# Kernel tuning notes

Hardware: AMD Instinct MI355X
Metric: run time of the kernel (lower is better)

The kernel has to match this reference:

```python
import jax, jax.numpy as jnp
import numpy as np

SEQ_LEN, IN_DIM = 120, 132
UNITS = (64, 128, 64)
N_LABELS = 101


def _lstm(x, W, U, b):
    """Keras-style LSTM with activation='relu', recurrent_activation='sigmoid'.
    x: (B,T,D), W: (D,4u), U: (u,4u), b: (4u,). Gate order i,f,c,o.
    Returns full hidden sequence (B,T,u)."""
    u = U.shape[0]
    # precompute input projections for all timesteps (big GEMM outside scan)
    xz = jnp.einsum('btd,dz->btz', x, W) + b  # (B,T,4u)

    def step(carry, z_t):
        h, c = carry
        z = z_t + h @ U  # (B,4u)
        i, f, g, o = jnp.split(z, 4, axis=-1)
        i = jax.nn.sigmoid(i)
        f = jax.nn.sigmoid(f)
        o = jax.nn.sigmoid(o)
        c = f * c + i * jax.nn.relu(g)
        h = o * jax.nn.relu(c)
        return (h, c), h

    B = x.shape[0]
    h0 = jnp.zeros((B, u), x.dtype)
    (_, _), hs = jax.lax.scan(step, (h0, h0), jnp.swapaxes(xz, 0, 1))
    return jnp.swapaxes(hs, 0, 1)  # (B,T,u)


def setup_inputs() -> dict:
    key = jax.random.key(0)
    ks = jax.random.split(key, 16)
    s = 0.05
    d = {'x': jax.random.normal(ks[0], (1024, SEQ_LEN, IN_DIM), jnp.float32)}
    in_dims = (IN_DIM,) + UNITS[:-1]
    for l, (din, u) in enumerate(zip(in_dims, UNITS), start=1):
        d[f'W{l}'] = jax.random.normal(ks[3 * l - 2], (din, 4 * u), jnp.float32) * s
        d[f'U{l}'] = jax.random.normal(ks[3 * l - 1], (u, 4 * u), jnp.float32) * s
        d[f'b{l}'] = jnp.zeros((4 * u,), jnp.float32)
    dense_dims = [(UNITS[-1], 64), (64, 32), (32, N_LABELS)]
    for l, (din, dout) in enumerate(dense_dims, start=1):
        d[f'Wd{l}'] = jax.random.normal(ks[9 + l], (din, dout), jnp.float32) * s
        d[f'bd{l}'] = jnp.zeros((dout,), jnp.float32)
    return d


def reference(x, W1, U1, b1, W2, U2, b2, W3, U3, b3,
              Wd1, bd1, Wd2, bd2, Wd3, bd3):
    h = _lstm(x, W1, U1, b1)          # (B,T,64)
    h = _lstm(h, W2, U2, b2)          # (B,T,128)
    h = _lstm(h, W3, U3, b3)[:, -1]   # return_sequences=False -> (B,64)
    h = jax.nn.relu(h @ Wd1 + bd1)    # (B,64)
    h = jax.nn.relu(h @ Wd2 + bd2)    # (B,32)
    return jax.nn.softmax(h @ Wd3 + bd3, axis=-1)  # (B,101)
```

## Files before the change

kernel.cpp:

```cpp
#include <hip/hip_runtime.h>
#include <math.h>

#define T_STEPS 120
#define BATCH   1024

typedef __attribute__((ext_vector_type(8))) short bf16x8;
typedef __attribute__((ext_vector_type(4))) float f32x4;
typedef unsigned short u16;

__device__ __forceinline__ unsigned split2(float f) {
    union { float f; unsigned u; } a; a.f = f;
    unsigned hi = a.u >> 16;
    union { float f; unsigned u; } h; h.u = a.u & 0xFFFF0000u;
    union { float f; unsigned u; } b; b.f = f - h.f;
    unsigned rr = b.u + 0x7FFFu + ((b.u >> 16) & 1);
    return (hi << 16) | (rr >> 16);
}

__device__ __forceinline__ short bf16rne(float f) {
    union { float f; unsigned u; } a; a.f = f;
    unsigned r = a.u + 0x7FFFu + ((a.u >> 16) & 1);
    return (short)(r >> 16);
}

__device__ __forceinline__ float fast_sigmoid(float x) {
    float e = __expf(-x);
    return __builtin_amdgcn_rcpf(1.f + e);
}

__device__ __forceinline__ void block_sync_lds() {
    asm volatile("s_waitcnt lgkmcnt(0)" ::: "memory");
    __builtin_amdgcn_sched_barrier(0);
    __builtin_amdgcn_s_barrier();
    __builtin_amdgcn_sched_barrier(0);
}

__global__ __launch_bounds__(256)
void xconv(const float* __restrict__ x, u16* __restrict__ xhi)
{
    int idx = blockIdx.x * 256 + threadIdx.x;
    int k   = idx % 144;
    int bt  = idx / 144;
    float f = (k < 132) ? x[(size_t)bt * 132 + k] : 0.f;
    xhi[idx] = (u16)(unsigned short)bf16rne(f);
}

template<int U, int KXD, int KTX, int KTAIL, bool XLO, bool WLO, bool LAST_ONLY>
__global__ __launch_bounds__(512, 1)
void lstm_fused(const u16* __restrict__ xhi, const u16* __restrict__ xlo,
                const float* __restrict__ W, int KIN,
                const float* __restrict__ Uw, const float* __restrict__ bias,
                u16* __restrict__ hhi, u16* __restrict__ hlo,
                float* __restrict__ hlast)
{
    constexpr int NZ  = 4 * U;
    constexpr int KTH = U / 32;
    constexpr int NB  = 16;
    constexpr int HPLANE = NB * U;
    constexpr int NGRP = U / 16;
    constexpr int XPSTRIDE = 20;
    static_assert(NGRP * 128 == 512, "4 h-waves + 4 x-waves");

    __shared__ u16 hsh[4 * HPLANE];
    __shared__ float xp[2 * NZ * XPSTRIDE];

    const int tid  = threadIdx.x;
    const int lane = tid & 63;
    const int wid  = tid >> 6;
    const int ln   = lane & 15;
    const int lq   = lane >> 4;
    const bool ish = (wid < NGRP);
    const int g    = ish ? wid : wid - NGRP;
    const int unit = g * 16 + ln;
    const int b0   = blockIdx.x * NB;

    if (ish) {
        bf16x8 bwu[4][KTH];
#pragma unroll
        for (int p = 0; p < 4; ++p)
#pragma unroll
            for (int kt = 0; kt < KTH; ++kt)
#pragma unroll
                for (int e = 0; e < 8; ++e) {
                    int k = kt * 32 + lq * 8 + e;
                    bwu[p][kt][e] = bf16rne(Uw[(size_t)k * NZ + p * U + unit]);
                }
        float breg[4];
#pragma unroll
        for (int p = 0; p < 4; ++p) breg[p] = bias[p * U + unit];

        u16* hw0 = hsh + ((unit >> 3) * NB + lq * 4) * 8 + (unit & 7);
        u16* hw1 = hw0 + 2 * HPLANE;
        float creg[4];
#pragma unroll
        for (int r = 0; r < 4; ++r) {
            creg[r] = 0.f;
            hw0[r * 8] = 0;
            hw0[HPLANE + r * 8] = 0;
        }

        const u16* hrd[2][KTH];
#pragma unroll
        for (int b = 0; b < 2; ++b)
#pragma unroll
            for (int kt = 0; kt < KTH; ++kt)
                hrd[b][kt] = hsh + b * 2 * HPLANE + ((kt * 4 + lq) * NB + ln) * 8;

        const float* xprd[2];
        xprd[0] = xp;
        xprd[1] = xp + (size_t)NZ * XPSTRIDE;

        size_t ho = ((size_t)(b0 + lq * 4) * T_STEPS) * U + unit;

        block_sync_lds();

#define HSTEP(CUR, OTH, tc)                                                     \
    {                                                                           \
        f32x4 xpv[4];                                                           \
        _Pragma("unroll")                                                       \
        for (int p = 0; p < 4; ++p)                                             \
            xpv[p] = *reinterpret_cast<const f32x4*>(                           \
                xprd[CUR] + (p * U + unit) * XPSTRIDE + lq * 4);                \
        f32x4 acc[4] = {};                                                      \
        _Pragma("unroll")                                                       \
        for (int kt = 0; kt < KTH; ++kt) {                                      \
            bf16x8 ahh = *reinterpret_cast<const bf16x8*>(hrd[CUR][kt]);        \
            bf16x8 ahl = *reinterpret_cast<const bf16x8*>(hrd[CUR][kt] + HPLANE); \
            _Pragma("unroll")                                                   \
            for (int p = 0; p < 4; ++p) {                                       \
                acc[p] = __builtin_amdgcn_mfma_f32_16x16x32_bf16(ahh, bwu[p][kt], acc[p], 0, 0, 0); \
                acc[p] = __builtin_amdgcn_mfma_f32_16x16x32_bf16(ahl, bwu[p][kt], acc[p], 0, 0, 0); \
            }                                                                   \
        }                                                                       \
        _Pragma("unroll")                                                       \
        for (int r = 0; r < 4; ++r) {                                           \
            float zi = acc[0][r] + xpv[0][r] + breg[0];                         \
            float zf = acc[1][r] + xpv[1][r] + breg[1];                         \
            float zg = acc[2][r] + xpv[2][r] + breg[2];                         \
            float zo = acc[3][r] + xpv[3][r] + breg[3];                         \
            float si = fast_sigmoid(zi);                                        \
            float sf = fast_sigmoid(zf);                                        \
            float gg = fmaxf(zg, 0.f);                                          \
            float so = fast_sigmoid(zo);                                        \
            float c  = sf * creg[r] + si * gg;                                  \
            creg[r] = c;                                                        \
            float h = so * fmaxf(c, 0.f);                                       \
            unsigned s = split2(h);                                             \
            u16* hw = (OTH) ? hw1 : hw0;                                        \
            hw[r * 8] = (u16)(s >> 16);                                         \
            hw[HPLANE + r * 8] = (u16)s;                                        \
            if constexpr (!LAST_ONLY) {                                         \
                size_t o = ho + (size_t)r * (T_STEPS * U) + (size_t)(tc) * U;   \
                hhi[o] = (u16)(s >> 16);                                        \
                if constexpr (WLO) hlo[o] = (u16)s;                             \
            } else {                                                            \
                if ((tc) == T_STEPS - 1)                                        \
                    hlast[(size_t)(b0 + lq * 4 + r) * U + unit] = h;            \
            }                                                                   \
        }                                                                       \
        block_sync_lds();                                                       \
    }

        for (int t = 0; t < T_STEPS; t += 2) {
            HSTEP(0, 1, t)
            HSTEP(1, 0, t + 1)
        }
#undef HSTEP
    } else {
        bf16x8 wxw[KTX][4];
#pragma unroll
        for (int kt = 0; kt < KTX; ++kt)
#pragma unroll
            for (int p = 0; p < 4; ++p)
#pragma unroll
                for (int e = 0; e < 8; ++e) {
                    int k = kt * 32 + lq * 8 + e;
                    wxw[kt][p][e] = (k < KIN) ? bf16rne(W[(size_t)k * NZ + p * U + unit])
                                              : (short)0;
                }

        const u16* pxh = xhi + ((size_t)(b0 + ln) * T_STEPS) * KXD + lq * 8;
        const u16* pxl = XLO ? (xlo + ((size_t)(b0 + ln) * T_STEPS) * KXD + lq * 8) : nullptr;

        float* xpw[2];
        xpw[0] = xp;
        xpw[1] = xp + (size_t)NZ * XPSTRIDE;

        bf16x8 xfh[KTX] = {}, xfl[KTX] = {};
#pragma unroll
        for (int kt = 0; kt < KTX; ++kt)
            if (kt < KTX - 1 || lq < KTAIL) {
                xfh[kt] = *reinterpret_cast<const bf16x8*>(pxh + kt * 32);
                if constexpr (XLO)
                    xfl[kt] = *reinterpret_cast<const bf16x8*>(pxl + kt * 32);
            }

        {
            f32x4 xacc[4] = {};
#pragma unroll
            for (int kt = 0; kt < KTX; ++kt)
#pragma unroll
                for (int p = 0; p < 4; ++p) {
                    xacc[p] = __builtin_amdgcn_mfma_f32_16x16x32_bf16(xfh[kt], wxw[kt][p], xacc[p], 0, 0, 0);
                    if constexpr (XLO)
                        xacc[p] = __builtin_amdgcn_mfma_f32_16x16x32_bf16(xfl[kt], wxw[kt][p], xacc[p], 0, 0, 0);
                }
#pragma unroll
            for (int p = 0; p < 4; ++p)
                *reinterpret_cast<f32x4*>(xpw[0] + (p * U + unit) * XPSTRIDE + lq * 4) = xacc[p];
            pxh += KXD; if constexpr (XLO) pxl += KXD;
#pragma unroll
            for (int kt = 0; kt < KTX; ++kt)
                if (kt < KTX - 1 || lq < KTAIL) {
                    xfh[kt] = *reinterpret_cast<const bf16x8*>(pxh + kt * 32);
                    if constexpr (XLO)
                        xfl[kt] = *reinterpret_cast<const bf16x8*>(pxl + kt * 32);
                }
        }

        block_sync_lds();

#define XSTEP(OTH, tc)                                                          \
    {                                                                           \
        if ((tc) + 1 < T_STEPS) {                                               \
            f32x4 xacc[4] = {};                                                 \
            _Pragma("unroll")                                                   \
            for (int kt = 0; kt < KTX; ++kt)                                    \
            _Pragma("unroll")                                                   \
            for (int p = 0; p < 4; ++p) {                                       \
                xacc[p] = __builtin_amdgcn_mfma_f32_16x16x32_bf16(xfh[kt], wxw[kt][p], xacc[p], 0, 0, 0); \
                if constexpr (XLO)                                              \
                    xacc[p] = __builtin_amdgcn_mfma_f32_16x16x32_bf16(xfl[kt], wxw[kt][p], xacc[p], 0, 0, 0); \
            }                                                                   \
            _Pragma("unroll")                                                   \
            for (int p = 0; p < 4; ++p)                                         \
                *reinterpret_cast<f32x4*>(xpw[OTH] + (p * U + unit) * XPSTRIDE + lq * 4) = xacc[p]; \
            if ((tc) + 2 < T_STEPS) {                                           \
                pxh += KXD; if constexpr (XLO) pxl += KXD;                      \
                _Pragma("unroll")                                               \
                for (int kt = 0; kt < KTX; ++kt)                                \
                    if (kt < KTX - 1 || lq < KTAIL) {                           \
                        xfh[kt] = *reinterpret_cast<const bf16x8*>(pxh + kt * 32); \
                        if constexpr (XLO)                                      \
                            xfl[kt] = *reinterpret_cast<const bf16x8*>(pxl + kt * 32); \
                    }                                                           \
            }                                                                   \
        }                                                                       \
        block_sync_lds();                                                       \
    }

        for (int t = 0; t < T_STEPS; t += 2) {
            XSTEP(1, t)
            XSTEP(0, t + 1)
        }
#undef XSTEP
    }
}

__global__ __launch_bounds__(512, 1)
void lstm_l2(const u16* __restrict__ xhi,
             const float* __restrict__ W,
             const float* __restrict__ Uw,
             const float* __restrict__ bias,
             u16* __restrict__ hhi, u16* __restrict__ hlo)
{
    constexpr int U = 128, NZ = 512, KTH = 4, NB = 16, KXD = 64, KTX = 2;
    constexpr int HPLANE = NB * U;
    __shared__ u16 hsh[4 * HPLANE];
    __shared__ u16 Wl[KXD * NZ];

    const int tid  = threadIdx.x;
    const int lane = tid & 63;
    const int wid  = tid >> 6;
    const int ln   = lane & 15;
    const int lq   = lane >> 4;
    const int unit = wid * 16 + ln;
    const int b0   = blockIdx.x * NB;

    for (int idx = tid; idx < KXD * NZ; idx += 512) {
        int k = idx >> 9, n = idx & (NZ - 1);
        Wl[((k >> 3) * NZ + n) * 8 + (k & 7)] = (u16)bf16rne(W[(size_t)k * NZ + n]);
    }

    bf16x8 bwu[4][KTH];
#pragma unroll
    for (int p = 0; p < 4; ++p)
#pragma unroll
        for (int kt = 0; kt < KTH; ++kt)
#pragma unroll
            for (int e = 0; e < 8; ++e) {
                int k = kt * 32 + lq * 8 + e;
                bwu[p][kt][e] = bf16rne(Uw[(size_t)k * NZ + p * U + unit]);
            }
    float breg[4];
#pragma unroll
    for (int p = 0; p < 4; ++p) breg[p] = bias[p * U + unit];

    u16* hw0 = hsh + ((unit >> 3) * NB + lq * 4) * 8 + (unit & 7);
    u16* hw1 = hw0 + 2 * HPLANE;
    float creg[4];
#pragma unroll
    for (int r = 0; r < 4; ++r) {
        creg[r] = 0.f;
        hw0[r * 8] = 0;
        hw0[HPLANE + r * 8] = 0;
    }

    const u16* hrd[2][KTH];
#pragma unroll
    for (int b = 0; b < 2; ++b)
#pragma unroll
        for (int kt = 0; kt < KTH; ++kt)
            hrd[b][kt] = hsh + b * 2 * HPLANE + ((kt * 4 + lq) * NB + ln) * 8;

    const u16* wb = Wl + ((size_t)lq * NZ + unit) * 8;

    const u16* pxh = xhi + ((size_t)(b0 + ln) * T_STEPS) * KXD + lq * 8;
    bf16x8 xfh[KTX];
#pragma unroll
    for (int kt = 0; kt < KTX; ++kt)
        xfh[kt] = *reinterpret_cast<const bf16x8*>(pxh + kt * 32);

    size_t ho = ((size_t)(b0 + lq * 4) * T_STEPS) * U + unit;

    block_sync_lds();

#define L2STEP(CUR, OTH, tc)                                                    \
    {                                                                           \
        f32x4 acc[4] = {};                                                      \
        _Pragma("unroll")                                                       \
        for (int kt = 0; kt < KTH; ++kt) {                                      \
            bf16x8 ahh = *reinterpret_cast<const bf16x8*>(hrd[CUR][kt]);        \
            bf16x8 ahl = *reinterpret_cast<const bf16x8*>(hrd[CUR][kt] + HPLANE); \
            _Pragma("unroll")                                                   \
            for (int p = 0; p < 4; ++p) {                                       \
                acc[p] = __builtin_amdgcn_mfma_f32_16x16x32_bf16(ahh, bwu[p][kt], acc[p], 0, 0, 0); \
                acc[p] = __builtin_amdgcn_mfma_f32_16x16x32_bf16(ahl, bwu[p][kt], acc[p], 0, 0, 0); \
            }                                                                   \
        }                                                                       \
        _Pragma("unroll")                                                       \
        for (int kt = 0; kt < KTX; ++kt)                                        \
        _Pragma("unroll")                                                       \
        for (int p = 0; p < 4; ++p) {                                           \
            bf16x8 wf = *reinterpret_cast<const bf16x8*>(wb + (kt * 4 * NZ + p * U) * 8); \
            acc[p] = __builtin_amdgcn_mfma_f32_16x16x32_bf16(xfh[kt], wf, acc[p], 0, 0, 0); \
        }                                                                       \
        if ((tc) + 1 < T_STEPS) {                                               \
            pxh += KXD;                                                         \
            _Pragma("unroll")                                                   \
            for (int kt = 0; kt < KTX; ++kt)                                    \
                xfh[kt] = *reinterpret_cast<const bf16x8*>(pxh + kt * 32);      \
        }                                                                       \
        _Pragma("unroll")                                                       \
        for (int r = 0; r < 4; ++r) {                                           \
            float si = fast_sigmoid(acc[0][r] + breg[0]);                       \
            float sf = fast_sigmoid(acc[1][r] + breg[1]);                       \
            float gg = fmaxf(acc[2][r] + breg[2], 0.f);                         \
            float so = fast_sigmoid(acc[3][r] + breg[3]);                       \
            float c  = sf * creg[r] + si * gg;                                  \
            creg[r] = c;                                                        \
            float h = so * fmaxf(c, 0.f);                                       \
            unsigned s = split2(h);                                             \
            u16* hw = (OTH) ? hw1 : hw0;                                        \
            hw[r * 8] = (u16)(s >> 16);                                         \
            hw[HPLANE + r * 8] = (u16)s;                                        \
            size_t o = ho + (size_t)r * (T_STEPS * U) + (size_t)(tc) * U;       \
            hhi[o] = (u16)(s >> 16);                                            \
            hlo[o] = (u16)s;                                                    \
        }                                                                       \
        block_sync_lds();                                                       \
    }

    for (int t = 0; t < T_STEPS; t += 2) {
        L2STEP(0, 1, t)
        L2STEP(1, 0, t + 1)
    }
#undef L2STEP
}

__global__ __launch_bounds__(256)
void dense_head(const float* __restrict__ h3,
                const float* __restrict__ Wd1, const float* __restrict__ bd1,
                const float* __restrict__ Wd2, const float* __restrict__ bd2,
                const float* __restrict__ Wd3, const float* __restrict__ bd3,
                float* __restrict__ out)
{
    __shared__ float s1[4][64];
    __shared__ float s2[4][32];
    const int w    = threadIdx.x >> 6;
    const int lane = threadIdx.x & 63;
    const int row  = blockIdx.x * 4 + w;

    float hval = h3[(size_t)row * 64 + lane];
    float a = bd1[lane];
#pragma unroll
    for (int k = 0; k < 64; ++k) {
        float hk = __shfl(hval, k, 64);
        a = fmaf(hk, Wd1[k * 64 + lane], a);
    }
    s1[w][lane] = fmaxf(a, 0.f);
    __syncthreads();

    if (lane < 32) {
        float a2 = bd2[lane];
#pragma unroll
        for (int k = 0; k < 64; ++k) a2 = fmaf(s1[w][k], Wd2[k * 32 + lane], a2);
        s2[w][lane] = fmaxf(a2, 0.f);
    }
    __syncthreads();

    float a0 = bd3[lane];
#pragma unroll
    for (int k = 0; k < 32; ++k) a0 = fmaf(s2[w][k], Wd3[k * 101 + lane], a0);
    float a1 = -INFINITY;
    if (lane < 37) {
        a1 = bd3[64 + lane];
#pragma unroll
        for (int k = 0; k < 32; ++k) a1 = fmaf(s2[w][k], Wd3[k * 101 + 64 + lane], a1);
    }

    float m = fmaxf(a0, a1);
#pragma unroll
    for (int off = 32; off > 0; off >>= 1) m = fmaxf(m, __shfl_xor(m, off, 64));
    float e0 = expf(a0 - m);
    float e1 = (lane < 37) ? expf(a1 - m) : 0.f;
    float s = e0 + e1;
#pragma unroll
    for (int off = 32; off > 0; off >>= 1) s += __shfl_xor(s, off, 64);

    out[(size_t)row * 101 + lane] = e0 / s;
    if (lane < 37) out[(size_t)row * 101 + 64 + lane] = e1 / s;
}

extern "C" void kernel_launch(void* const* d_in, const int* in_sizes, int n_in,
                              void* d_out, int out_size, void* d_ws, size_t ws_size,
                              hipStream_t stream) {
    const float* x   = (const float*)d_in[0];
    const float* W1  = (const float*)d_in[1];
    const float* U1  = (const float*)d_in[2];
    const float* b1  = (const float*)d_in[3];
    const float* W2  = (const float*)d_in[4];
    const float* U2  = (const float*)d_in[5];
    const float* b2  = (const float*)d_in[6];
    const float* W3  = (const float*)d_in[7];
    const float* U3  = (const float*)d_in[8];
    const float* b3  = (const float*)d_in[9];
    const float* Wd1 = (const float*)d_in[10];
    const float* bd1 = (const float*)d_in[11];
    const float* Wd2 = (const float*)d_in[12];
    const float* bd2 = (const float*)d_in[13];
    const float* Wd3 = (const float*)d_in[14];
    const float* bd3 = (const float*)d_in[15];

    u16* ws16 = (u16*)d_ws;
    u16* xhi  = ws16;
    u16* h2hi = ws16;
    u16* h2lo = h2hi + 15728640;
    u16* h1hi = ws16 + 35389440;
    float* h3 = (float*)(ws16 + 51118080);

    xconv<<<(BATCH * T_STEPS * 144) / 256, 256, 0, stream>>>(x, xhi);
    lstm_fused<64, 144, 5, 2, false, false, false><<<64, 512, 0, stream>>>(
        xhi, nullptr, W1, 132, U1, b1, h1hi, nullptr, nullptr);
    lstm_l2<<<64, 512, 0, stream>>>(h1hi, W2, U2, b2, h2hi, h2lo);
    lstm_fused<64, 128, 4, 4, true, true, true><<<64, 512, 0, stream>>>(
        h2hi, h2lo, W3, 128, U3, b3, nullptr, nullptr, h3);
    dense_head<<<BATCH / 4, 256, 0, stream>>>(h3, Wd1, bd1, Wd2, bd2, Wd3, bd3,
                                              (float*)d_out);
}
```

Before: 507.6 us.

## Hoist input projections into standalone GEMM and drop split-bf16 precision

Moves the input projection of LSTM layers 1 and 3 out of the recurrent kernel into a separate MFMA GEMM that writes bf16 pre-activations in a step-major tiled layout. The recurrent kernel then only does the h@U recurrence, with 8 waves covering two 16-row batch tiles per block over 32 blocks. The hi/lo split-bf16 trick for h is removed in all layers, halving the recurrent MFMAs and h stores. In exchange the change adds a large xz round-trip through memory and lowers numerical precision (bf16 h and bf16 stored projections).

Result: slower. 538.7 us (+6.1%).

```diff
diff --git a/kernel.cpp b/kernel.cpp
--- a/kernel.cpp
+++ b/kernel.cpp
@@ -6,21 +6,20 @@
 
 typedef __attribute__((ext_vector_type(8))) short bf16x8;
 typedef __attribute__((ext_vector_type(4))) float f32x4;
+typedef __attribute__((ext_vector_type(4))) unsigned short us4;
 typedef unsigned short u16;
 
-__device__ __forceinline__ unsigned split2(float f) {
-    union { float f; unsigned u; } a; a.f = f;
-    unsigned hi = a.u >> 16;
-    union { float f; unsigned u; } h; h.u = a.u & 0xFFFF0000u;
-    union { float f; unsigned u; } b; b.f = f - h.f;
-    unsigned rr = b.u + 0x7FFFu + ((b.u >> 16) & 1);
-    return (hi << 16) | (rr >> 16);
-}
-
-__device__ __forceinline__ short bf16rne(float f) {
+__device__ __forceinline__ int gsw(int r) { return (r & 7) ^ ((r >> 3) & 1); }
+
+__device__ __forceinline__ u16 bf16rne(float f) {
     union { float f; unsigned u; } a; a.f = f;
     unsigned r = a.u + 0x7FFFu + ((a.u >> 16) & 1);
-    return (short)(r >> 16);
+    return (u16)(r >> 16);
+}
+
+__device__ __forceinline__ float bf2f(u16 v) {
+    union { unsigned u; float f; } a; a.u = ((unsigned)v) << 16;
+    return a.f;
 }
 
 __device__ __forceinline__ float fast_sigmoid(float x) {
@@ -35,109 +34,210 @@
     __builtin_amdgcn_sched_barrier(0);
 }
 
-__global__ __launch_bounds__(256)
-void xconv(const float* __restrict__ x, u16* __restrict__ xhi)
+template<bool AF32>
+__global__ __launch_bounds__(256, 2)
+void gemm_xz(const void* __restrict__ Av, const float* __restrict__ Bw,
+             u16* __restrict__ XZF, int N, int K)
 {
-    int idx = blockIdx.x * 256 + threadIdx.x;
-    int k   = idx % 144;
-    int bt  = idx / 144;
-    float f = (k < 132) ? x[(size_t)bt * 132 + k] : 0.f;
-    xhi[idx] = (u16)(unsigned short)bf16rne(f);
-}
-
-template<int U, int KXD, int KTX, int KTAIL, bool XLO, bool WLO, bool LAST_ONLY>
+    constexpr int BM = 128, BN = 64, BK = 64;
+    __shared__ u16 Ah[BM * BK];
+    __shared__ u16 Bh[BN * BK];
+
+    const float* Af = (const float*)Av;
+    const u16*   Ab = (const u16*)Av;
+
+    const int tid  = threadIdx.x;
+    const int lane = tid & 63;
+    const int wv   = tid >> 6;
+    const int wm   = wv & 1;
+    const int wn   = wv >> 1;
+    const int m0   = blockIdx.x * BM;
+    const int n0   = blockIdx.y * BN;
+
+    f32x4 acc[4][2] = {};
+
+    const int ktiles = (K + BK - 1) / BK;
+    for (int kt = 0; kt < ktiles; ++kt) {
+        const int kb = kt * BK;
+        __syncthreads();
+
+        {
+            const int f4   = tid & 15;
+            const int sub  = (f4 & 1) * 4;
+            const int k8   = f4 >> 1;
+            const int kidx = kb + f4 * 4;
+            const bool kok = (kidx < K);
+            for (int rd = 0; rd < 8; ++rd) {
+                int m  = rd * 16 + (tid >> 4);
+                int gm = m0 + m;
+                us4 hh;
+                if (kok) {
+                    if constexpr (AF32) {
+                        float4 v = *reinterpret_cast<const float4*>(
+                            &Af[(size_t)gm * K + kidx]);
+                        hh.x = bf16rne(v.x); hh.y = bf16rne(v.y);
+                        hh.z = bf16rne(v.z); hh.w = bf16rne(v.w);
+                    } else {
+                        hh = *reinterpret_cast<const us4*>(
+                            &Ab[(size_t)gm * K + kidx]);
+                    }
+                } else {
+                    hh.x = 0; hh.y = 0; hh.z = 0; hh.w = 0;
+                }
+                int off = m * 64 + ((k8 ^ gsw(m & 15)) * 8) + sub;
+                *reinterpret_cast<us4*>(&Ah[off]) = hh;
+            }
+        }
+        {
+#pragma unroll
+            for (int i = 0; i < 2; ++i) {
+                int u  = tid + i * 256;
+                int n  = u & 63;
+                int k8 = u >> 6;
+                u16 th[8];
+#pragma unroll
+                for (int e = 0; e < 8; ++e) {
+                    int k = kb + k8 * 8 + e;
+                    th[e] = (k < K) ? bf16rne(Bw[(size_t)k * N + n0 + n]) : (u16)0;
+                }
+                us4 h0, h1;
+                h0.x = th[0]; h0.y = th[1]; h0.z = th[2]; h0.w = th[3];
+                h1.x = th[4]; h1.y = th[5]; h1.z = th[6]; h1.w = th[7];
+                int off = n * 64 + ((k8 ^ gsw(n & 15)) * 8);
+                *reinterpret_cast<us4*>(&Bh[off])     = h0;
+                *reinterpret_cast<us4*>(&Bh[off + 4]) = h1;
+            }
+        }
+        __syncthreads();
+
+        const int row = lane & 15;
+        const int kq  = lane >> 4;
+        const int gr  = gsw(row);
+#pragma unroll
+        for (int ks = 0; ks < 2; ++ks) {
+            const int k8 = ks * 4 + kq;
+            bf16x8 bh[2];
+#pragma unroll
+            for (int ni = 0; ni < 2; ++ni) {
+                int n = wn * 32 + ni * 16 + row;
+                bh[ni] = *reinterpret_cast<const bf16x8*>(&Bh[n * 64 + ((k8 ^ gr) * 8)]);
+            }
+#pragma unroll
+            for (int mi = 0; mi < 4; ++mi) {
+                int m = wm * 64 + mi * 16 + row;
+                bf16x8 ah = *reinterpret_cast<const bf16x8*>(&Ah[m * 64 + ((k8 ^ gr) * 8)]);
+#pragma unroll
+                for (int ni = 0; ni < 2; ++ni)
+                    acc[mi][ni] = __builtin_amdgcn_mfma_f32_16x16x32_bf16(ah, bh[ni], acc[mi][ni], 0, 0, 0);
+            }
+        }
+    }
+
+    const int col = lane & 15;
+    const int rq  = (lane >> 4) * 4;
+#pragma unroll
+    for (int mi = 0; mi < 4; ++mi) {
+#pragma unroll
+        for (int r = 0; r < 4; ++r) {
+            int gm = m0 + wm * 64 + mi * 16 + rq + r;
+            int b  = gm / T_STEPS;
+            int t  = gm - b * T_STEPS;
+#pragma unroll
+            for (int ni = 0; ni < 2; ++ni) {
+                int n = n0 + wn * 32 + ni * 16 + col;
+                size_t addr = (((((size_t)t * 64 + (b >> 4)) * 16 + (n >> 4)) * 64)
+                               + ((b & 15) >> 2) * 16 + (n & 15)) * 4 + (b & 3);
+                XZF[addr] = bf16rne(acc[mi][ni][r]);
+            }
+        }
+    }
+}
+
+template<bool LAST_ONLY>
 __global__ __launch_bounds__(512, 1)
-void lstm_fused(const u16* __restrict__ xhi, const u16* __restrict__ xlo,
-                const float* __restrict__ W, int KIN,
-                const float* __restrict__ Uw, const float* __restrict__ bias,
-                u16* __restrict__ hhi, u16* __restrict__ hlo,
+void lstm_rec64(const u16* __restrict__ XZF,
+                const float* __restrict__ Uw,
+                const float* __restrict__ bias,
+                u16* __restrict__ hout,
                 float* __restrict__ hlast)
 {
-    constexpr int NZ  = 4 * U;
-    constexpr int KTH = U / 32;
-    constexpr int NB  = 16;
-    constexpr int HPLANE = NB * U;
-    constexpr int NGRP = U / 16;
-    constexpr int XPSTRIDE = 20;
-    static_assert(NGRP * 128 == 512, "4 h-waves + 4 x-waves");
-
-    __shared__ u16 hsh[4 * HPLANE];
-    __shared__ float xp[2 * NZ * XPSTRIDE];
+    constexpr int U = 64, NZ = 256, KTH = 2;
+    constexpr int HPLANE = 16 * U;
+    constexpr size_t XSTEP = (size_t)64 * 16 * 64 * 4;
+
+    __shared__ u16 hsh[2][2][HPLANE];
 
     const int tid  = threadIdx.x;
     const int lane = tid & 63;
     const int wid  = tid >> 6;
     const int ln   = lane & 15;
     const int lq   = lane >> 4;
-    const bool ish = (wid < NGRP);
-    const int g    = ish ? wid : wid - NGRP;
-    const int unit = g * 16 + ln;
-    const int b0   = blockIdx.x * NB;
-
-    if (ish) {
-        bf16x8 bwu[4][KTH];
-#pragma unroll
-        for (int p = 0; p < 4; ++p)
-#pragma unroll
-            for (int kt = 0; kt < KTH; ++kt)
-#pragma unroll
-                for (int e = 0; e < 8; ++e) {
-                    int k = kt * 32 + lq * 8 + e;
-                    bwu[p][kt][e] = bf16rne(Uw[(size_t)k * NZ + p * U + unit]);
-                }
-        float breg[4];
-#pragma unroll
-        for (int p = 0; p < 4; ++p) breg[p] = bias[p * U + unit];
-
-        u16* hw0 = hsh + ((unit >> 3) * NB + lq * 4) * 8 + (unit & 7);
-        u16* hw1 = hw0 + 2 * HPLANE;
-        float creg[4];
-#pragma unroll
-        for (int r = 0; r < 4; ++r) {
-            creg[r] = 0.f;
-            hw0[r * 8] = 0;
-            hw0[HPLANE + r * 8] = 0;
-        }
-
-        const u16* hrd[2][KTH];
-#pragma unroll
-        for (int b = 0; b < 2; ++b)
-#pragma unroll
-            for (int kt = 0; kt < KTH; ++kt)
-                hrd[b][kt] = hsh + b * 2 * HPLANE + ((kt * 4 + lq) * NB + ln) * 8;
-
-        const float* xprd[2];
-        xprd[0] = xp;
-        xprd[1] = xp + (size_t)NZ * XPSTRIDE;
-
-        size_t ho = ((size_t)(b0 + lq * 4) * T_STEPS) * U + unit;
-
-        block_sync_lds();
-
-#define HSTEP(CUR, OTH, tc)                                                     \
+    const int ug   = wid & 3;
+    const int bh   = wid >> 2;
+    const int unit = ug * 16 + ln;
+    const int bkw  = blockIdx.x * 2 + bh;
+    const int b0   = bkw * 16;
+
+    bf16x8 bwu[4][KTH];
+#pragma unroll
+    for (int p = 0; p < 4; ++p)
+#pragma unroll
+        for (int kt = 0; kt < KTH; ++kt)
+#pragma unroll
+            for (int e = 0; e < 8; ++e) {
+                int k = kt * 32 + lq * 8 + e;
+                bwu[p][kt][e] = (short)bf16rne(Uw[(size_t)k * NZ + p * U + unit]);
+            }
+    float breg[4];
+#pragma unroll
+    for (int p = 0; p < 4; ++p) breg[p] = bias[p * U + unit];
+
+    u16* hw0 = &hsh[0][bh][((unit >> 3) * 16 + lq * 4) * 8 + (unit & 7)];
+    u16* hw1 = &hsh[1][bh][((unit >> 3) * 16 + lq * 4) * 8 + (unit & 7)];
+    float creg[4];
+#pragma unroll
+    for (int r = 0; r < 4; ++r) { creg[r] = 0.f; hw0[r * 8] = 0; }
+
+    const u16* hrd[2][KTH];
+#pragma unroll
+    for (int b = 0; b < 2; ++b)
+#pragma unroll
+        for (int kt = 0; kt < KTH; ++kt)
+            hrd[b][kt] = &hsh[b][bh][((kt * 4 + lq) * 16 + ln) * 8];
+
+    const u16* pxz = XZF + (((size_t)0 * 64 + bkw) * 16) * 256 + lane * 4;
+    us4 xzv[4];
+#pragma unroll
+    for (int p = 0; p < 4; ++p)
+        xzv[p] = *reinterpret_cast<const us4*>(pxz + ((size_t)p * 4 + ug) * 256);
+
+    block_sync_lds();
+
+#define RSTEP(CUR, OTH, tc)                                                     \
     {                                                                           \
-        f32x4 xpv[4];                                                           \
-        _Pragma("unroll")                                                       \
-        for (int p = 0; p < 4; ++p)                                             \
-            xpv[p] = *reinterpret_cast<const f32x4*>(                           \
-                xprd[CUR] + (p * U + unit) * XPSTRIDE + lq * 4);                \
         f32x4 acc[4] = {};                                                      \
         _Pragma("unroll")                                                       \
         for (int kt = 0; kt < KTH; ++kt) {                                      \
-            bf16x8 ahh = *reinterpret_cast<const bf16x8*>(hrd[CUR][kt]);        \
-            bf16x8 ahl = *reinterpret_cast<const bf16x8*>(hrd[CUR][kt] + HPLANE); \
+            bf16x8 ah = *reinterpret_cast<const bf16x8*>(hrd[CUR][kt]);         \
             _Pragma("unroll")                                                   \
-            for (int p = 0; p < 4; ++p) {                                       \
-                acc[p] = __builtin_amdgcn_mfma_f32_16x16x32_bf16(ahh, bwu[p][kt], acc[p], 0, 0, 0); \
-                acc[p] = __builtin_amdgcn_mfma_f32_16x16x32_bf16(ahl, bwu[p][kt], acc[p], 0, 0, 0); \
-            }                                                                   \
+            for (int p = 0; p < 4; ++p)                                         \
+                acc[p] = __builtin_amdgcn_mfma_f32_16x16x32_bf16(ah, bwu[p][kt], acc[p], 0, 0, 0); \
+        }                                                                       \
+        us4 xcur[4];                                                            \
+        _Pragma("unroll")                                                       \
+        for (int p = 0; p < 4; ++p) xcur[p] = xzv[p];                           \
+        if ((tc) + 1 < T_STEPS) {                                               \
+            pxz += XSTEP;                                                       \
+            _Pragma("unroll")                                                   \
+            for (int p = 0; p < 4; ++p)                                         \
+                xzv[p] = *reinterpret_cast<const us4*>(pxz + ((size_t)p * 4 + ug) * 256); \
         }                                                                       \
         _Pragma("unroll")                                                       \
         for (int r = 0; r < 4; ++r) {                                           \
-            float zi = acc[0][r] + xpv[0][r] + breg[0];                         \
-            float zf = acc[1][r] + xpv[1][r] + breg[1];                         \
-            float zg = acc[2][r] + xpv[2][r] + breg[2];                         \
-            float zo = acc[3][r] + xpv[3][r] + breg[3];                         \
+            float zi = acc[0][r] + bf2f(xcur[0][r]) + breg[0];                  \
+            float zf = acc[1][r] + bf2f(xcur[1][r]) + breg[1];                  \
+            float zg = acc[2][r] + bf2f(xcur[2][r]) + breg[2];                  \
+            float zo = acc[3][r] + bf2f(xcur[3][r]) + breg[3];                  \
             float si = fast_sigmoid(zi);                                        \
             float sf = fast_sigmoid(zf);                                        \
             float gg = fmaxf(zg, 0.f);                                          \
@@ -145,14 +245,10 @@
             float c  = sf * creg[r] + si * gg;                                  \
             creg[r] = c;                                                        \
             float h = so * fmaxf(c, 0.f);                                       \
-            unsigned s = split2(h);                                             \
-            u16* hw = (OTH) ? hw1 : hw0;                                        \
-            hw[r * 8] = (u16)(s >> 16);                                         \
-            hw[HPLANE + r * 8] = (u16)s;                                        \
+            u16 hb = bf16rne(h);                                                \
+            ((OTH) ? hw1 : hw0)[r * 8] = hb;                                    \
             if constexpr (!LAST_ONLY) {                                         \
-                size_t o = ho + (size_t)r * (T_STEPS * U) + (size_t)(tc) * U;   \
-                hhi[o] = (u16)(s >> 16);                                        \
-                if constexpr (WLO) hlo[o] = (u16)s;                             \
+                hout[((size_t)(b0 + lq * 4 + r) * T_STEPS + (tc)) * U + unit] = hb; \
             } else {                                                            \
                 if ((tc) == T_STEPS - 1)                                        \
                     hlast[(size_t)(b0 + lq * 4 + r) * U + unit] = h;            \
@@ -161,100 +257,11 @@
         block_sync_lds();                                                       \
     }
 
-        for (int t = 0; t < T_STEPS; t += 2) {
-            HSTEP(0, 1, t)
-            HSTEP(1, 0, t + 1)
-        }
-#undef HSTEP
-    } else {
-        bf16x8 wxw[KTX][4];
-#pragma unroll
-        for (int kt = 0; kt < KTX; ++kt)
-#pragma unroll
-            for (int p = 0; p < 4; ++p)
-#pragma unroll
-                for (int e = 0; e < 8; ++e) {
-                    int k = kt * 32 + lq * 8 + e;
-                    wxw[kt][p][e] = (k < KIN) ? bf16rne(W[(size_t)k * NZ + p * U + unit])
-                                              : (short)0;
-                }
-
-        const u16* pxh = xhi + ((size_t)(b0 + ln) * T_STEPS) * KXD + lq * 8;
-        const u16* pxl = XLO ? (xlo + ((size_t)(b0 + ln) * T_STEPS) * KXD + lq * 8) : nullptr;
-
-        float* xpw[2];
-        xpw[0] = xp;
-        xpw[1] = xp + (size_t)NZ * XPSTRIDE;
-
-        bf16x8 xfh[KTX] = {}, xfl[KTX] = {};
-#pragma unroll
-        for (int kt = 0; kt < KTX; ++kt)
-            if (kt < KTX - 1 || lq < KTAIL) {
-                xfh[kt] = *reinterpret_cast<const bf16x8*>(pxh + kt * 32);
-                if constexpr (XLO)
-                    xfl[kt] = *reinterpret_cast<const bf16x8*>(pxl + kt * 32);
-            }
-
-        {
-            f32x4 xacc[4] = {};
-#pragma unroll
-            for (int kt = 0; kt < KTX; ++kt)
-#pragma unroll
-                for (int p = 0; p < 4; ++p) {
-                    xacc[p] = __builtin_amdgcn_mfma_f32_16x16x32_bf16(xfh[kt], wxw[kt][p], xacc[p], 0, 0, 0);
-                    if constexpr (XLO)
-                        xacc[p] = __builtin_amdgcn_mfma_f32_16x16x32_bf16(xfl[kt], wxw[kt][p], xacc[p], 0, 0, 0);
-                }
-#pragma unroll
-            for (int p = 0; p < 4; ++p)
-                *reinterpret_cast<f32x4*>(xpw[0] + (p * U + unit) * XPSTRIDE + lq * 4) = xacc[p];
-            pxh += KXD; if constexpr (XLO) pxl += KXD;
-#pragma unroll
-            for (int kt = 0; kt < KTX; ++kt)
-                if (kt < KTX - 1 || lq < KTAIL) {
-                    xfh[kt] = *reinterpret_cast<const bf16x8*>(pxh + kt * 32);
-                    if constexpr (XLO)
-                        xfl[kt] = *reinterpret_cast<const bf16x8*>(pxl + kt * 32);
-                }
-        }
-
-        block_sync_lds();
-
-#define XSTEP(OTH, tc)                                                          \
-    {                                                                           \
-        if ((tc) + 1 < T_STEPS) {                                               \
-            f32x4 xacc[4] = {};                                                 \
-            _Pragma("unroll")                                                   \
-            for (int kt = 0; kt < KTX; ++kt)                                    \
-            _Pragma("unroll")                                                   \
-            for (int p = 0; p < 4; ++p) {                                       \
-                xacc[p] = __builtin_amdgcn_mfma_f32_16x16x32_bf16(xfh[kt], wxw[kt][p], xacc[p], 0, 0, 0); \
-                if constexpr (XLO)                                              \
-                    xacc[p] = __builtin_amdgcn_mfma_f32_16x16x32_bf16(xfl[kt], wxw[kt][p], xacc[p], 0, 0, 0); \
-            }                                                                   \
-            _Pragma("unroll")                                                   \
-            for (int p = 0; p < 4; ++p)                                         \
-                *reinterpret_cast<f32x4*>(xpw[OTH] + (p * U + unit) * XPSTRIDE + lq * 4) = xacc[p]; \
-            if ((tc) + 2 < T_STEPS) {                                           \
-                pxh += KXD; if constexpr (XLO) pxl += KXD;                      \
-                _Pragma("unroll")                                               \
-                for (int kt = 0; kt < KTX; ++kt)                                \
-                    if (kt < KTX - 1 || lq < KTAIL) {                           \
-                        xfh[kt] = *reinterpret_cast<const bf16x8*>(pxh + kt * 32); \
-                        if constexpr (XLO)                                      \
-                            xfl[kt] = *reinterpret_cast<const bf16x8*>(pxl + kt * 32); \
-                    }                                                           \
-            }                                                                   \
-        }                                                                       \
-        block_sync_lds();                                                       \
-    }
-
-        for (int t = 0; t < T_STEPS; t += 2) {
-            XSTEP(1, t)
-            XSTEP(0, t + 1)
-        }
-#undef XSTEP
-    }
+    for (int t = 0; t < T_STEPS; t += 2) {
+        RSTEP(0, 1, t)
+        RSTEP(1, 0, t + 1)
+    }
+#undef RSTEP
 }
 
 __global__ __launch_bounds__(512, 1)
@@ -262,7 +269,7 @@
              const float* __restrict__ W,
              const float* __restrict__ Uw,
              const float* __restrict__ bias,
-             u16* __restrict__ hhi, u16* __restrict__ hlo)
+             u16* __restrict__ hhi)
 {
     constexpr int U = 128, NZ = 512, KTH = 4, NB = 16, KXD = 64, KTX = 2;
     constexpr int HPLANE = NB * U;
@@ -279,7 +286,7 @@
 
     for (int idx = tid; idx < KXD * NZ; idx += 512) {
         int k = idx >> 9, n = idx & (NZ - 1);
-        Wl[((k >> 3) * NZ + n) * 8 + (k & 7)] = (u16)bf16rne(W[(size_t)k * NZ + n]);
+        Wl[((k >> 3) * NZ + n) * 8 + (k & 7)] = bf16rne(W[(size_t)k * NZ + n]);
     }
 
     bf16x8 bwu[4][KTH];
@@ -290,7 +297,7 @@
 #pragma unroll
             for (int e = 0; e < 8; ++e) {
                 int k = kt * 32 + lq * 8 + e;
-                bwu[p][kt][e] = bf16rne(Uw[(size_t)k * NZ + p * U + unit]);
+                bwu[p][kt][e] = (short)bf16rne(Uw[(size_t)k * NZ + p * U + unit]);
             }
     float breg[4];
 #pragma unroll
@@ -331,18 +338,15 @@
         _Pragma("unroll")                                                       \
         for (int kt = 0; kt < KTH; ++kt) {                                      \
             bf16x8 ahh = *reinterpret_cast<const bf16x8*>(hrd[CUR][kt]);        \
-            bf16x8 ahl = *reinterpret_cast<const bf16x8*>(hrd[CUR][kt] + HPLANE); \
             _Pragma("unroll")                                                   \
-            for (int p = 0; p < 4; ++p) {                                       \
+            for (int p = 0; p < 4; ++p)                                         \
                 acc[p] = __builtin_amdgcn_mfma_f32_16x16x32_bf16(ahh, bwu[p][kt], acc[p], 0, 0, 0); \
-                acc[p] = __builtin_amdgcn_mfma_f32_16x16x32_bf16(ahl, bwu[p][kt], acc[p], 0, 0, 0); \
-            }                                                                   \
         }                                                                       \
         _Pragma("unroll")                                                       \
         for (int kt = 0; kt < KTX; ++kt)                                        \
         _Pragma("unroll")                                                       \
         for (int p = 0; p < 4; ++p) {                                           \
-            bf16x8 wf = *reinterpret_cast<const bf16x8*>(wb + (kt * 4 * NZ + p * U) * 8); \
+            bf16x8 wf = *reinterpret_cast<const bf16x8*>(wb + ((size_t)kt * 4 * NZ + p * U) * 8); \
             acc[p] = __builtin_amdgcn_mfma_f32_16x16x32_bf16(xfh[kt], wf, acc[p], 0, 0, 0); \
         }                                                                       \
         if ((tc) + 1 < T_STEPS) {                                               \
@@ -360,13 +364,11 @@
             float c  = sf * creg[r] + si * gg;                                  \
             creg[r] = c;                                                        \
             float h = so * fmaxf(c, 0.f);                                       \
-            unsigned s = split2(h);                                             \
+            u16 hb = bf16rne(h);                                                \
             u16* hw = (OTH) ? hw1 : hw0;                                        \
-            hw[r * 8] = (u16)(s >> 16);                                         \
-            hw[HPLANE + r * 8] = (u16)s;                                        \
-            size_t o = ho + (size_t)r * (T_STEPS * U) + (size_t)(tc) * U;       \
-            hhi[o] = (u16)(s >> 16);                                            \
-            hlo[o] = (u16)s;                                                    \
+            hw[r * 8] = hb;                                                     \
+            hw[HPLANE + r * 8] = hb;  \
+            hhi[ho + (size_t)r * (T_STEPS * U) + (size_t)(tc) * U] = hb;        \
         }                                                                       \
         block_sync_lds();                                                       \
     }
@@ -453,18 +455,16 @@
     const float* bd3 = (const float*)d_in[15];
 
     u16* ws16 = (u16*)d_ws;
-    u16* xhi  = ws16;
-    u16* h2hi = ws16;
-    u16* h2lo = h2hi + 15728640;
-    u16* h1hi = ws16 + 35389440;
-    float* h3 = (float*)(ws16 + 51118080);
-
-    xconv<<<(BATCH * T_STEPS * 144) / 256, 256, 0, stream>>>(x, xhi);
-    lstm_fused<64, 144, 5, 2, false, false, false><<<64, 512, 0, stream>>>(
-        xhi, nullptr, W1, 132, U1, b1, h1hi, nullptr, nullptr);
-    lstm_l2<<<64, 512, 0, stream>>>(h1hi, W2, U2, b2, h2hi, h2lo);
-    lstm_fused<64, 128, 4, 4, true, true, true><<<64, 512, 0, stream>>>(
-        h2hi, h2lo, W3, 128, U3, b3, nullptr, nullptr, h3);
+    u16* xzf  = ws16;
+    u16* h1   = ws16 + 31457280;
+    u16* h2   = h1 + 7864320;
+    float* h3 = (float*)(ws16 + 55050240);
+
+    gemm_xz<true><<<dim3(960, 4), 256, 0, stream>>>(x, W1, xzf, 256, 132);
+    lstm_rec64<false><<<32, 512, 0, stream>>>(xzf, U1, b1, h1, nullptr);
+    lstm_l2<<<64, 512, 0, stream>>>(h1, W2, U2, b2, h2);
+    gemm_xz<false><<<dim3(960, 4), 256, 0, stream>>>(h2, W3, xzf, 256, 128);
+    lstm_rec64<true><<<32, 512, 0, stream>>>(xzf, U3, b3, nullptr, h3);
     dense_head<<<BATCH / 4, 256, 0, stream>>>(h3, Wd1, bd1, Wd2, bd2, Wd3, bd3,
                                               (float*)d_out);
 }
```
